# Kernel tuning notes

Hardware: AMD Instinct MI355X
Metric: run time of the kernel (lower is better)

The kernel has to match this reference:

```python
import jax, jax.numpy as jnp
import numpy as np

N = 50000   # number of 'link' nodes
E = 800000  # edges per relation
H = 64      # h_dim

def setup_inputs() -> dict:
    key = jax.random.key(0)
    ks = jax.random.split(key, 9)
    return dict(
        h=jax.random.normal(ks[0], (N, H), jnp.float32),
        feat1=jax.random.normal(ks[1], (E, H), jnp.float32),
        feat2=jax.random.normal(ks[2], (E, H), jnp.float32),
        W1=jax.random.normal(ks[3], (2 * H, H), jnp.float32) / np.sqrt(2.0 * H).astype(np.float32),
        b1=jnp.zeros((H,), jnp.float32),
        W2=jax.random.normal(ks[4], (2 * H, H), jnp.float32) / np.sqrt(2.0 * H).astype(np.float32),
        b2=jnp.zeros((H,), jnp.float32),
        src1=jax.random.randint(ks[5], (E,), 0, N, jnp.int32),
        dst1=jax.random.randint(ks[6], (E,), 0, N, jnp.int32),
        src2=jax.random.randint(ks[7], (E,), 0, N, jnp.int32),
        dst2=jax.random.randint(ks[8], (E,), 0, N, jnp.int32),
    )

def _agg(h, src, dst, feat):
    # e_mul_u: edge feat * source node h, then sum-reduce to destination nodes
    return jax.ops.segment_sum(feat * h[src], dst, num_segments=N)

def reference(h, feat1, feat2, W1, b1, W2, b2, src1, dst1, src2, dst2):
    # n_layer = 2 message-passing steps, each with its own Linear(2H, H)
    for W, b in ((W1, b1), (W2, b2)):
        a1 = _agg(h, src1, dst1, feat1)          # [N, H] connect_to aggregate
        a2 = _agg(h, src2, dst2, feat2)          # [N, H] connected_by aggregate
        h_ = jnp.concatenate([a1, a2], axis=-1)  # cross-reducer concat -> [N, 2H]
        h_ = jax.nn.relu(h_ @ W + b)             # Linear + ReLU
        h = h + h_                               # residual update
    return h
```

## Files before the change

### kernel.cpp

```cpp
#include <hip/hip_runtime.h>

#define N_NODES 50000
#define HDIM 64
#define E_EDGES 800000
#define SCAN_BLK 1024
#define NPART ((N_NODES + SCAN_BLK - 1) / SCAN_BLK)
#define CHUNK 128
#define SEG_WAVES ((E_EDGES + CHUNK - 1) / CHUNK)

__device__ __forceinline__ float lane_bcast(float v, int l) {
    return __int_as_float(__builtin_amdgcn_readlane(__float_as_int(v), l));
}


__global__ void __launch_bounds__(256) hist_kernel(
        const int* __restrict__ dst1, const int* __restrict__ dst2,
        int* __restrict__ cnt1, int* __restrict__ cnt2) {
    const int* dst = blockIdx.y ? dst2 : dst1;
    int* cnt       = blockIdx.y ? cnt2 : cnt1;
    int e = blockIdx.x * 256 + threadIdx.x;
    if (e < E_EDGES) atomicAdd(&cnt[dst[e]], 1);
}

__global__ void __launch_bounds__(SCAN_BLK) partial_kernel(
        const int* __restrict__ cnt1, const int* __restrict__ cnt2,
        int* __restrict__ part) {
    const int* cnt = blockIdx.y ? cnt2 : cnt1;
    __shared__ int red[16];
    const int t = blockIdx.x * SCAN_BLK + threadIdx.x;
    int v = (t < N_NODES) ? cnt[t] : 0;
#pragma unroll
    for (int s = 32; s >= 1; s >>= 1) v += __shfl_xor(v, s);
    if ((threadIdx.x & 63) == 0) red[threadIdx.x >> 6] = v;
    __syncthreads();
    if (threadIdx.x == 0) {
        int ssum = 0;
#pragma unroll
        for (int i = 0; i < 16; ++i) ssum += red[i];
        part[blockIdx.y * NPART + blockIdx.x] = ssum;
    }
}

__global__ void __launch_bounds__(64) scanp_kernel(
        const int* __restrict__ part, int* __restrict__ pofs) {
    const int r = blockIdx.y;
    const int t = threadIdx.x;
    int v = (t < NPART) ? part[r * NPART + t] : 0;
    const int orig = v;
#pragma unroll
    for (int s = 1; s < 64; s <<= 1) {
        int u = __shfl_up(v, s);
        if (t >= s) v += u;
    }
    if (t < NPART) pofs[r * NPART + t] = v - orig;
}

__global__ void __launch_bounds__(SCAN_BLK) fill_kernel(
        const int* __restrict__ cnt1, const int* __restrict__ cnt2,
        const int* __restrict__ pofs,
        int* __restrict__ off1, int* __restrict__ off2,
        int* __restrict__ cur1, int* __restrict__ cur2) {
    const int* cnt = blockIdx.y ? cnt2 : cnt1;
    int* off       = blockIdx.y ? off2 : off1;
    int* cur       = blockIdx.y ? cur2 : cur1;

    __shared__ int lds[SCAN_BLK];
    const int t = threadIdx.x;
    const int gid = blockIdx.x * SCAN_BLK + t;
    const int c = (gid < N_NODES) ? cnt[gid] : 0;
    lds[t] = c;
    __syncthreads();
    for (int s = 1; s < SCAN_BLK; s <<= 1) {
        int v = (t >= s) ? lds[t - s] : 0;
        __syncthreads();
        lds[t] += v;
        __syncthreads();
    }
    const int excl = lds[t] - c + pofs[blockIdx.y * NPART + blockIdx.x];
    if (gid < N_NODES) { off[gid] = excl; cur[gid] = excl; }
    if (gid == 0 && blockIdx.x == 0) off[N_NODES] = E_EDGES;
}

__global__ void __launch_bounds__(256) scatter_kernel(
        const int* __restrict__ src1, const int* __restrict__ dst1,
        const int* __restrict__ src2, const int* __restrict__ dst2,
        int* __restrict__ cur1, int* __restrict__ cur2,
        int2* __restrict__ pairs1, int2* __restrict__ pairs2) {
    const int* src = blockIdx.y ? src2 : src1;
    const int* dst = blockIdx.y ? dst2 : dst1;
    int* cur       = blockIdx.y ? cur2 : cur1;
    int2* pairs    = blockIdx.y ? pairs2 : pairs1;
    int e = blockIdx.x * 256 + threadIdx.x;
    if (e >= E_EDGES) return;
    int pos = atomicAdd(&cur[dst[e]], 1);
    pairs[pos] = make_int2(src[e], e);
}


__global__ void __launch_bounds__(256) agg_seg_kernel(
        const float* __restrict__ h,
        const float* __restrict__ feat1, const float* __restrict__ feat2,
        const int* __restrict__ off1, const int* __restrict__ off2,
        const int2* __restrict__ pairs1, const int2* __restrict__ pairs2,
        float* __restrict__ a1, float* __restrict__ a2) {
    const float* feat = blockIdx.y ? feat2  : feat1;
    const int* off    = blockIdx.y ? off2   : off1;
    const int2* pairs = blockIdx.y ? pairs2 : pairs1;
    float* agg        = blockIdx.y ? a2     : a1;

    const int lane = threadIdx.x & 63;
    const int wv = blockIdx.x * 4 + (threadIdx.x >> 6);
    if (wv >= SEG_WAVES) return;

    const int C0 = wv * CHUNK;
    int C1 = C0 + CHUNK;
    if (C1 >= E_EDGES) C1 = E_EDGES + 1;

    int lo = 0, hi = N_NODES;
    while (lo < hi) {
        int mid = (lo + hi) >> 1;
        if (off[mid] < C0) lo = mid + 1; else hi = mid;
    }
    int n = lo;
    if (n >= N_NODES) return;

    int s = off[n];
    while (s >= C0 && s < C1) {
        const int e = off[n + 1];
        float acc = 0.f;
        int i = s;
        for (; i + 4 <= e; i += 4) {
            int2 p0 = pairs[i];
            int2 p1 = pairs[i + 1];
            int2 p2 = pairs[i + 2];
            int2 p3 = pairs[i + 3];
            const float f0 = feat[((size_t)__builtin_amdgcn_readfirstlane(p0.y) << 6) + lane];
            const float g0 = h   [((size_t)__builtin_amdgcn_readfirstlane(p0.x) << 6) + lane];
            const float f1 = feat[((size_t)__builtin_amdgcn_readfirstlane(p1.y) << 6) + lane];
            const float g1 = h   [((size_t)__builtin_amdgcn_readfirstlane(p1.x) << 6) + lane];
            const float f2 = feat[((size_t)__builtin_amdgcn_readfirstlane(p2.y) << 6) + lane];
            const float g2 = h   [((size_t)__builtin_amdgcn_readfirstlane(p2.x) << 6) + lane];
            const float f3 = feat[((size_t)__builtin_amdgcn_readfirstlane(p3.y) << 6) + lane];
            const float g3 = h   [((size_t)__builtin_amdgcn_readfirstlane(p3.x) << 6) + lane];
            acc = fmaf(f0, g0, acc);
            acc = fmaf(f1, g1, acc);
            acc = fmaf(f2, g2, acc);
            acc = fmaf(f3, g3, acc);
        }
        for (; i < e; ++i) {
            int2 p = pairs[i];
            const float f = feat[((size_t)__builtin_amdgcn_readfirstlane(p.y) << 6) + lane];
            const float g = h   [((size_t)__builtin_amdgcn_readfirstlane(p.x) << 6) + lane];
            acc = fmaf(f, g, acc);
        }
        agg[((size_t)n << 6) + lane] = acc;
        if (++n >= N_NODES) break;
        s = e;
    }
}


__global__ void __launch_bounds__(256, 2) mlp_kernel(
        const float* __restrict__ h_in,
        const float* __restrict__ a1,
        const float* __restrict__ a2,
        const float* __restrict__ W,
        const float* __restrict__ b,
        float* __restrict__ h_out) {
    const int lane = threadIdx.x & 63;

    float w1r[HDIM], w2r[HDIM];
#pragma unroll
    for (int k = 0; k < HDIM; ++k) w1r[k] = W[k * HDIM + lane];
#pragma unroll
    for (int k = 0; k < HDIM; ++k) w2r[k] = W[(HDIM + k) * HDIM + lane];
    const float bias = b[lane];

    const int wv = blockIdx.x * 4 + (threadIdx.x >> 6);
    const int stride = gridDim.x * 4;
    for (int node = wv; node < N_NODES; node += stride) {
        const size_t base = (size_t)node << 6;
        const float x1 = a1[base + lane];
        const float x2 = a2[base + lane];
        float acc1 = bias, acc2 = 0.f;
#pragma unroll
        for (int k = 0; k < HDIM; ++k) {
            acc1 = fmaf(lane_bcast(x1, k), w1r[k], acc1);
            acc2 = fmaf(lane_bcast(x2, k), w2r[k], acc2);
        }
        const float r = acc1 + acc2;
        h_out[base + lane] = h_in[base + lane] + fmaxf(r, 0.f);
    }
}


__global__ void __launch_bounds__(256) agg_atomic_kernel(
        const float* __restrict__ h,
        const float* __restrict__ feat,
        const int* __restrict__ src,
        const int* __restrict__ dst,
        float* __restrict__ agg) {
    const int tid  = blockIdx.x * 256 + threadIdx.x;
    const int lane = threadIdx.x & 63;
    const int sub  = lane >> 4;
    const int q    = lane & 15;
    const int e    = (tid >> 6) * 4 + sub;
    if (e >= E_EDGES) return;
    const int s = src[e];
    const int d = dst[e];
    const float4 f  = *(const float4*)&feat[(size_t)e * HDIM + q * 4];
    const float4 hv = *(const float4*)&h[(size_t)s * HDIM + q * 4];
    float* p = &agg[(size_t)d * HDIM + q * 4];
    atomicAdd(p + 0, f.x * hv.x);
    atomicAdd(p + 1, f.y * hv.y);
    atomicAdd(p + 2, f.z * hv.z);
    atomicAdd(p + 3, f.w * hv.w);
}

extern "C" void kernel_launch(void* const* d_in, const int* in_sizes, int n_in,
                              void* d_out, int out_size, void* d_ws, size_t ws_size,
                              hipStream_t stream) {
    const float* h     = (const float*)d_in[0];
    const float* feat1 = (const float*)d_in[1];
    const float* feat2 = (const float*)d_in[2];
    const float* W1    = (const float*)d_in[3];
    const float* b1    = (const float*)d_in[4];
    const float* W2    = (const float*)d_in[5];
    const float* b2    = (const float*)d_in[6];
    const int*   src1  = (const int*)d_in[7];
    const int*   dst1  = (const int*)d_in[8];
    const int*   src2  = (const int*)d_in[9];
    const int*   dst2  = (const int*)d_in[10];

    float* out = (float*)d_out;

    float* a1   = (float*)d_ws;
    float* a2   = a1 + (size_t)N_NODES * HDIM;
    int*   cnt1 = (int*)(a2 + (size_t)N_NODES * HDIM);
    int*   cnt2 = cnt1 + N_NODES;
    int*   off1 = cnt2 + N_NODES;
    int*   off2 = off1 + (N_NODES + 1);
    int*   cur1 = off2 + (N_NODES + 1);
    int*   cur2 = cur1 + N_NODES;
    int*   part = cur2 + N_NODES;
    int*   pofs = part + 2 * NPART;
    int2*  pairs1 = (int2*)(pofs + 2 * NPART);
    int2*  pairs2 = pairs1 + E_EDGES;

    const size_t needed = (char*)(pairs2 + E_EDGES) - (char*)d_ws;

    const int eBlocks   = (E_EDGES + 255) / 256;
    const int segBlocks = (SEG_WAVES + 3) / 4;

    if (ws_size >= needed) {
        hipMemsetAsync(cnt1, 0, 2 * (size_t)N_NODES * sizeof(int), stream);
        hist_kernel<<<dim3(eBlocks, 2), 256, 0, stream>>>(dst1, dst2, cnt1, cnt2);
        partial_kernel<<<dim3(NPART, 2), SCAN_BLK, 0, stream>>>(cnt1, cnt2, part);
        scanp_kernel<<<dim3(1, 2), 64, 0, stream>>>(part, pofs);
        fill_kernel<<<dim3(NPART, 2), SCAN_BLK, 0, stream>>>(
            cnt1, cnt2, pofs, off1, off2, cur1, cur2);
        scatter_kernel<<<dim3(eBlocks, 2), 256, 0, stream>>>(
            src1, dst1, src2, dst2, cur1, cur2, pairs1, pairs2);

        agg_seg_kernel<<<dim3(segBlocks, 2), 256, 0, stream>>>(
            h, feat1, feat2, off1, off2, pairs1, pairs2, a1, a2);
        mlp_kernel<<<1024, 256, 0, stream>>>(h, a1, a2, W1, b1, out);

        agg_seg_kernel<<<dim3(segBlocks, 2), 256, 0, stream>>>(
            out, feat1, feat2, off1, off2, pairs1, pairs2, a1, a2);
        mlp_kernel<<<1024, 256, 0, stream>>>(out, a1, a2, W2, b2, out);
    } else {
        const size_t aggBytes = 2 * (size_t)N_NODES * HDIM * sizeof(float);
        const int atomBlocks = (E_EDGES + 15) / 16;

        hipMemsetAsync(d_ws, 0, aggBytes, stream);
        agg_atomic_kernel<<<atomBlocks, 256, 0, stream>>>(h, feat1, src1, dst1, a1);
        agg_atomic_kernel<<<atomBlocks, 256, 0, stream>>>(h, feat2, src2, dst2, a2);
        mlp_kernel<<<1024, 256, 0, stream>>>(h, a1, a2, W1, b1, out);

        hipMemsetAsync(d_ws, 0, aggBytes, stream);
        agg_atomic_kernel<<<atomBlocks, 256, 0, stream>>>(out, feat1, src1, dst1, a1);
        agg_atomic_kernel<<<atomBlocks, 256, 0, stream>>>(out, feat2, src2, dst2, a2);
        mlp_kernel<<<1024, 256, 0, stream>>>(out, a1, a2, W2, b2, out);
    }
}
```

Baseline: 890.6 us.

## Precompute wave start nodes, stage pairs in LDS, split edges across lane groups

```diff
diff --git a/kernel.cpp b/kernel.cpp
--- a/kernel.cpp
+++ b/kernel.cpp
@@ -96,64 +96,79 @@
     pairs[pos] = make_int2(src[e], e);
 }
 
+__global__ void __launch_bounds__(256) wstart_kernel(
+        const int* __restrict__ off1, const int* __restrict__ off2,
+        int* __restrict__ wstart1, int* __restrict__ wstart2) {
+    const int* off = blockIdx.y ? off2 : off1;
+    int* wstart    = blockIdx.y ? wstart2 : wstart1;
+    const int w = blockIdx.x * 256 + threadIdx.x;
+    if (w >= SEG_WAVES) return;
+    const int C0 = w * CHUNK;
+    int lo = 0, hi = N_NODES;
+    while (lo < hi) {
+        int mid = (lo + hi) >> 1;
+        if (off[mid] < C0) lo = mid + 1; else hi = mid;
+    }
+    wstart[w] = lo;
+}
+
 
 __global__ void __launch_bounds__(256) agg_seg_kernel(
         const float* __restrict__ h,
         const float* __restrict__ feat1, const float* __restrict__ feat2,
         const int* __restrict__ off1, const int* __restrict__ off2,
         const int2* __restrict__ pairs1, const int2* __restrict__ pairs2,
+        const int* __restrict__ wstart1, const int* __restrict__ wstart2,
         float* __restrict__ a1, float* __restrict__ a2) {
-    const float* feat = blockIdx.y ? feat2  : feat1;
-    const int* off    = blockIdx.y ? off2   : off1;
-    const int2* pairs = blockIdx.y ? pairs2 : pairs1;
-    float* agg        = blockIdx.y ? a2     : a1;
-
-    const int lane = threadIdx.x & 63;
-    const int wv = blockIdx.x * 4 + (threadIdx.x >> 6);
+    const float* feat  = blockIdx.y ? feat2   : feat1;
+    const int* off     = blockIdx.y ? off2    : off1;
+    const int2* pairs  = blockIdx.y ? pairs2  : pairs1;
+    const int* wstart  = blockIdx.y ? wstart2 : wstart1;
+    float* agg         = blockIdx.y ? a2      : a1;
+
+    __shared__ int2 plds[4][CHUNK];
+
+    const int tid  = threadIdx.x;
+    const int lane = tid & 63;
+    const int wsl  = tid >> 6;
+    const int g    = lane >> 4;
+    const int q    = lane & 15;
+    const int wv   = blockIdx.x * 4 + wsl;
     if (wv >= SEG_WAVES) return;
 
     const int C0 = wv * CHUNK;
     int C1 = C0 + CHUNK;
     if (C1 >= E_EDGES) C1 = E_EDGES + 1;
 
-    int lo = 0, hi = N_NODES;
-    while (lo < hi) {
-        int mid = (lo + hi) >> 1;
-        if (off[mid] < C0) lo = mid + 1; else hi = mid;
-    }
-    int n = lo;
+    plds[wsl][lane]      = pairs[C0 + lane];
+    plds[wsl][lane + 64] = pairs[C0 + lane + 64];
+
+    int n = wstart[wv];
     if (n >= N_NODES) return;
 
     int s = off[n];
     while (s >= C0 && s < C1) {
         const int e = off[n + 1];
-        float acc = 0.f;
-        int i = s;
-        for (; i + 4 <= e; i += 4) {
-            int2 p0 = pairs[i];
-            int2 p1 = pairs[i + 1];
-            int2 p2 = pairs[i + 2];
-            int2 p3 = pairs[i + 3];
-            const float f0 = feat[((size_t)__builtin_amdgcn_readfirstlane(p0.y) << 6) + lane];
-            const float g0 = h   [((size_t)__builtin_amdgcn_readfirstlane(p0.x) << 6) + lane];
-            const float f1 = feat[((size_t)__builtin_amdgcn_readfirstlane(p1.y) << 6) + lane];
-            const float g1 = h   [((size_t)__builtin_amdgcn_readfirstlane(p1.x) << 6) + lane];
-            const float f2 = feat[((size_t)__builtin_amdgcn_readfirstlane(p2.y) << 6) + lane];
-            const float g2 = h   [((size_t)__builtin_amdgcn_readfirstlane(p2.x) << 6) + lane];
-            const float f3 = feat[((size_t)__builtin_amdgcn_readfirstlane(p3.y) << 6) + lane];
-            const float g3 = h   [((size_t)__builtin_amdgcn_readfirstlane(p3.x) << 6) + lane];
-            acc = fmaf(f0, g0, acc);
-            acc = fmaf(f1, g1, acc);
-            acc = fmaf(f2, g2, acc);
-            acc = fmaf(f3, g3, acc);
+        float4 acc = make_float4(0.f, 0.f, 0.f, 0.f);
+#pragma unroll 2
+        for (int i = s + g; i < e; i += 4) {
+            int2 p;
+            if (i < C0 + CHUNK) p = plds[wsl][i - C0];
+            else                p = pairs[i];
+            const float4 f  = *(const float4*)&feat[((size_t)p.y << 6) + (q << 2)];
+            const float4 hv = *(const float4*)&h[((size_t)p.x << 6) + (q << 2)];
+            acc.x = fmaf(f.x, hv.x, acc.x);
+            acc.y = fmaf(f.y, hv.y, acc.y);
+            acc.z = fmaf(f.z, hv.z, acc.z);
+            acc.w = fmaf(f.w, hv.w, acc.w);
         }
-        for (; i < e; ++i) {
-            int2 p = pairs[i];
-            const float f = feat[((size_t)__builtin_amdgcn_readfirstlane(p.y) << 6) + lane];
-            const float g = h   [((size_t)__builtin_amdgcn_readfirstlane(p.x) << 6) + lane];
-            acc = fmaf(f, g, acc);
+        acc.x += __shfl_xor(acc.x, 16); acc.y += __shfl_xor(acc.y, 16);
+        acc.z += __shfl_xor(acc.z, 16); acc.w += __shfl_xor(acc.w, 16);
+        acc.x += __shfl_xor(acc.x, 32); acc.y += __shfl_xor(acc.y, 32);
+        acc.z += __shfl_xor(acc.z, 32); acc.w += __shfl_xor(acc.w, 32);
+        if (lane < 16) {
+            *(float4*)&agg[((size_t)n << 6) + (q << 2)] = acc;
         }
-        agg[((size_t)n << 6) + lane] = acc;
         if (++n >= N_NODES) break;
         s = e;
     }
@@ -244,13 +259,16 @@
     int*   cur2 = cur1 + N_NODES;
     int*   part = cur2 + N_NODES;
     int*   pofs = part + 2 * NPART;
-    int2*  pairs1 = (int2*)(pofs + 2 * NPART);
+    int*   wstart1 = pofs + 2 * NPART;
+    int*   wstart2 = wstart1 + SEG_WAVES;
+    int2*  pairs1 = (int2*)(wstart2 + SEG_WAVES);
     int2*  pairs2 = pairs1 + E_EDGES;
 
     const size_t needed = (char*)(pairs2 + E_EDGES) - (char*)d_ws;
 
     const int eBlocks   = (E_EDGES + 255) / 256;
     const int segBlocks = (SEG_WAVES + 3) / 4;
+    const int wsBlocks  = (SEG_WAVES + 255) / 256;
 
     if (ws_size >= needed) {
         hipMemsetAsync(cnt1, 0, 2 * (size_t)N_NODES * sizeof(int), stream);
@@ -261,13 +279,15 @@
             cnt1, cnt2, pofs, off1, off2, cur1, cur2);
         scatter_kernel<<<dim3(eBlocks, 2), 256, 0, stream>>>(
             src1, dst1, src2, dst2, cur1, cur2, pairs1, pairs2);
+        wstart_kernel<<<dim3(wsBlocks, 2), 256, 0, stream>>>(
+            off1, off2, wstart1, wstart2);
 
         agg_seg_kernel<<<dim3(segBlocks, 2), 256, 0, stream>>>(
-            h, feat1, feat2, off1, off2, pairs1, pairs2, a1, a2);
+            h, feat1, feat2, off1, off2, pairs1, pairs2, wstart1, wstart2, a1, a2);
         mlp_kernel<<<1024, 256, 0, stream>>>(h, a1, a2, W1, b1, out);
 
         agg_seg_kernel<<<dim3(segBlocks, 2), 256, 0, stream>>>(
-            out, feat1, feat2, off1, off2, pairs1, pairs2, a1, a2);
+            out, feat1, feat2, off1, off2, pairs1, pairs2, wstart1, wstart2, a1, a2);
         mlp_kernel<<<1024, 256, 0, stream>>>(out, a1, a2, W2, b2, out);
     } else {
         const size_t aggBytes = 2 * (size_t)N_NODES * HDIM * sizeof(float);
```

Result: faster. 838.9 us (-5.8%).
